# Optimization experiments

Measured on AMD Instinct MI355X. Metric: run time of the kernel, lower is better.

## Reference

```python
import jax, jax.numpy as jnp
import numpy as np

CHUNK = 1024  # mirrors torch chunk_size; keeps per-step intermediate bounded


def _chunked_min_dist(source, target):
    # source: [N, d], target: [M, d] -> [N] min squared distance to target
    n, d = source.shape
    chunks = source.reshape(n // CHUNK, CHUNK, d)

    def step(chunk):
        # diff: [CHUNK, M, d]; dist: [CHUNK, M]
        diff = chunk[:, None, :] - target[None, :, :]
        dist = jnp.sum(diff * diff, axis=-1)
        return jnp.min(dist, axis=1)

    mins = jax.lax.map(step, chunks)  # [n//CHUNK, CHUNK]
    return mins.reshape(n)


def setup_inputs() -> dict:
    key = jax.random.key(0)
    k1, k2 = jax.random.split(key)
    pred = jax.random.normal(k1, (32768, 3), dtype=jnp.float32)
    target = jax.random.normal(k2, (32768, 3), dtype=jnp.float32)
    return {"pred": pred, "target": target}


def reference(pred, target):
    min_pred_to_target = _chunked_min_dist(pred, target)
    min_target_to_pred = _chunked_min_dist(target, pred)
    # reduction='mean'
    return min_pred_to_target.mean() + min_target_to_pred.mean()
```

## Files before the change

### kernel.cpp

```cpp
#include <hip/hip_runtime.h>

#define NPTS 32768
#define G 32
#define NCELL (G*G*G)
#define SSTR (NCELL + 1)
#define RANGE 4.5f
#define CELLW 0.28125f

typedef unsigned int u32;


__device__ __forceinline__ int cell_of(float v) {
    int c = (int)floorf((v + RANGE) * (G / (2.0f * RANGE)));
    return min(max(c, 0), G - 1);
}
__device__ __forceinline__ float cell_lo(int i) {
    return fmaf((float)i, CELLW, -RANGE);
}

__global__ __launch_bounds__(256)
void hist_k(const float* __restrict__ pred, const float* __restrict__ targ,
            u32* __restrict__ cnt, u32* __restrict__ strag_cnt,
            float* __restrict__ out) {
    int i = blockIdx.x * 256 + threadIdx.x;
    if (i == 0) { *out = 0.0f; *strag_cnt = 0u; }
    int cloud = i >> 15, k = i & (NPTS - 1);
    const float* p = cloud ? targ : pred;
    float x = p[3*k], y = p[3*k+1], z = p[3*k+2];
    int c = (cell_of(z) * G + cell_of(y)) * G + cell_of(x);
    atomicAdd(&cnt[cloud * NCELL + c], 1u);
}

__global__ __launch_bounds__(1024)
void scan_k(const u32* __restrict__ cnt, u32* __restrict__ S, u32* __restrict__ cursor) {
    int cloud = blockIdx.x;
    const u32* c = cnt + cloud * NCELL;
    u32* s   = S + cloud * SSTR;
    u32* cur = cursor + cloud * NCELL;
    __shared__ u32 wt[16];
    int t = threadIdx.x, lane = t & 63, wave = t >> 6;

    u32 loc[32], run = 0;
    #pragma unroll
    for (int k = 0; k < 32; ++k) { loc[k] = run; run += c[32 * t + k]; }
    u32 inc = run;
    #pragma unroll
    for (int off = 1; off < 64; off <<= 1) {
        u32 nv = __shfl_up(inc, off, 64);
        if (lane >= off) inc += nv;
    }
    if (lane == 63) wt[wave] = inc;
    __syncthreads();
    if (t == 0) {
        u32 a = 0;
        #pragma unroll
        for (int w = 0; w < 16; ++w) { u32 v = wt[w]; wt[w] = a; a += v; }
    }
    __syncthreads();
    u32 tb = wt[wave] + (inc - run);
    #pragma unroll
    for (int k = 0; k < 32; ++k) {
        u32 v = tb + loc[k];
        s[32 * t + k] = v; cur[32 * t + k] = v;
    }
    if (t == 1023) s[NCELL] = NPTS;
}

__global__ __launch_bounds__(256)
void scatter_k(const float* __restrict__ pred, const float* __restrict__ targ,
               u32* __restrict__ cursor,
               float4* __restrict__ sortedA, float4* __restrict__ sortedB) {
    int i = blockIdx.x * 256 + threadIdx.x;
    int cloud = i >> 15, k = i & (NPTS - 1);
    const float* p = cloud ? targ : pred;
    float x = p[3*k], y = p[3*k+1], z = p[3*k+2];
    int c = (cell_of(z) * G + cell_of(y)) * G + cell_of(x);
    u32 pos = atomicAdd(&cursor[cloud * NCELL + c], 1u);
    (cloud ? sortedB : sortedA)[pos] = make_float4(x, y, z, 0.0f);
}

__device__ __forceinline__ float box_bound(int cx, int cy, int cz, float4 q, int R) {
    float bd = 3.4e38f;
    if (cx - R > 0)     bd = fminf(bd, q.x - cell_lo(cx - R));
    if (cx + R < G - 1) bd = fminf(bd, cell_lo(cx + R + 1) - q.x);
    if (cy - R > 0)     bd = fminf(bd, q.y - cell_lo(cy - R));
    if (cy + R < G - 1) bd = fminf(bd, cell_lo(cy + R + 1) - q.y);
    if (cz - R > 0)     bd = fminf(bd, q.z - cell_lo(cz - R));
    if (cz + R < G - 1) bd = fminf(bd, cell_lo(cz + R + 1) - q.z);
    return bd;
}

__global__ __launch_bounds__(256, 8)
void query_dense(const float4* __restrict__ sortedA, const float4* __restrict__ sortedB,
                 const u32* __restrict__ Sall, u32* __restrict__ strag_cnt,
                 u32* __restrict__ strag_list, float* __restrict__ out) {
    int tid = blockIdx.x * 256 + threadIdx.x;
    int sub = tid & 7;
    int qi = tid >> 3;
    int cloud = qi >> 15, k = qi & (NPTS - 1);
    const float4* Q = cloud ? sortedB : sortedA;
    const float4* T = cloud ? sortedA : sortedB;
    const u32* s = Sall + (cloud ^ 1) * SSTR;

    float4 q = Q[k];
    int cx = cell_of(q.x), cy = cell_of(q.y), cz = cell_of(q.z);
    int x0 = max(cx - 1, 0), x1 = min(cx + 1, G - 1);
    float best = 3.4e38f;

    int cbc = (cz * G + cy) * G;
    u32 cbeg = s[cbc + x0], cend = s[cbc + x1 + 1];
    u32 rb[9], re[9];
    #pragma unroll
    for (int i = 0; i < 9; ++i) {
        int dy = (i % 3) - 1, dz = (i / 3) - 1;
        int Y = cy + dy, Z = cz + dz;
        rb[i] = 0; re[i] = 0;
        if (i != 4 && (unsigned)Y < G && (unsigned)Z < G) {
            int cb = (Z * G + Y) * G;
            rb[i] = s[cb + x0]; re[i] = s[cb + x1 + 1];
        }
    }

    auto scan_seg = [&](u32 beg, u32 end) {
        for (u32 e = beg + sub; e < end; e += 8) {
            float4 t = T[e];
            float dx = q.x - t.x, dy = q.y - t.y, dz = q.z - t.z;
            best = fminf(best, fmaf(dx, dx, fmaf(dy, dy, dz * dz)));
        }
    };
    auto group_min = [&]() {
        best = fminf(best, __shfl_xor(best, 1, 64));
        best = fminf(best, __shfl_xor(best, 2, 64));
        best = fminf(best, __shfl_xor(best, 4, 64));
    };

    scan_seg(cbeg, cend);
    group_min();

    #pragma unroll
    for (int i = 0; i < 9; ++i) {
        if (i == 4) continue;
        int dy = (i % 3) - 1, dz = (i / 3) - 1;
        int Y = cy + dy, Z = cz + dz;
        if ((unsigned)Y >= G || (unsigned)Z >= G) continue;
        float ey = dy > 0 ? cell_lo(Y) - q.y : q.y - cell_lo(Y + 1);
        float ez = dz > 0 ? cell_lo(Z) - q.z : q.z - cell_lo(Z + 1);
        if (dy == 0) ey = 0.0f;
        if (dz == 0) ez = 0.0f;
        float mind2 = fmaf(ey, ey, ez * ez);
        if (mind2 < best) scan_seg(rb[i], re[i]);
    }
    group_min();

    float bd = box_bound(cx, cy, cz, q, 1);
    if (best > bd * bd) {
        if (sub == 0) {
            u32 slot = atomicAdd(strag_cnt, 1u);
            strag_list[slot] = (u32)qi;
        }
        best = 0.0f;
    }

    float v = best * 0.125f;
    #pragma unroll
    for (int off = 1; off < 64; off <<= 1)
        v += __shfl_xor(v, off, 64);
    __shared__ float wsum[4];
    int lane = threadIdx.x & 63, wave = threadIdx.x >> 6;
    if (lane == 0) wsum[wave] = v;
    __syncthreads();
    if (threadIdx.x == 0)
        atomicAdd(out, (wsum[0] + wsum[1] + wsum[2] + wsum[3]) * (1.0f / NPTS));
}

__global__ __launch_bounds__(256, 8)
void query_strag(const float4* __restrict__ sortedA, const float4* __restrict__ sortedB,
                 const u32* __restrict__ Sall, const u32* __restrict__ strag_cnt,
                 const u32* __restrict__ strag_list, float* __restrict__ out) {
    u32 n = *strag_cnt;
    int lane = threadIdx.x & 63;
    u32 wid = (blockIdx.x * 256 + threadIdx.x) >> 6;
    u32 nw = (gridDim.x * 256) >> 6;

    for (u32 idx = wid; idx < n; idx += nw) {
        u32 qi = strag_list[idx];
        int cloud = qi >> 15, k = qi & (NPTS - 1);
        const float4* Q = cloud ? sortedB : sortedA;
        const float4* T = cloud ? sortedA : sortedB;
        const u32* s = Sall + (cloud ^ 1) * SSTR;

        float4 q = Q[k];
        int cx = cell_of(q.x), cy = cell_of(q.y), cz = cell_of(q.z);
        int xlo = max(cx - 4, 0), xhi = min(cx + 4, G - 1);
        float best = 3.4e38f;

        u32 rb0 = 0, re0 = 0, rb1 = 0, re1 = 0;
        {
            int Z = cz + lane / 9 - 4, Y = cy + lane % 9 - 4;
            if ((unsigned)Z < G && (unsigned)Y < G) {
                int cb = (Z * G + Y) * G;
                rb0 = s[cb + xlo]; re0 = s[cb + xhi + 1];
            }
        }
        if (lane < 17) {
            int ri = lane + 64;
            int Z = cz + ri / 9 - 4, Y = cy + ri % 9 - 4;
            if ((unsigned)Z < G && (unsigned)Y < G) {
                int cb = (Z * G + Y) * G;
                rb1 = s[cb + xlo]; re1 = s[cb + xhi + 1];
            }
        }
        for (u32 e = rb0; e < re0; ++e) {
            float4 t = T[e];
            float dx = q.x - t.x, dy = q.y - t.y, dz = q.z - t.z;
            best = fminf(best, fmaf(dx, dx, fmaf(dy, dy, dz * dz)));
        }
        for (u32 e = rb1; e < re1; ++e) {
            float4 t = T[e];
            float dx = q.x - t.x, dy = q.y - t.y, dz = q.z - t.z;
            best = fminf(best, fmaf(dx, dx, fmaf(dy, dy, dz * dz)));
        }
        #pragma unroll
        for (int off = 1; off < 64; off <<= 1)
            best = fminf(best, __shfl_xor(best, off, 64));

        float bd4 = box_bound(cx, cy, cz, q, 4);
        if (best > bd4 * bd4) {
            auto d2 = [&](float4 t) {
                float dx = q.x - t.x, dy = q.y - t.y, dz = q.z - t.z;
                return fmaf(dx, dx, fmaf(dy, dy, dz * dz));
            };
            float a0 = 3.4e38f, a1 = 3.4e38f, a2 = 3.4e38f, a3 = 3.4e38f;
            #pragma unroll 2
            for (int blk = 0; blk < NPTS / 512; ++blk) {
                u32 base = (u32)lane + (u32)blk * 512u;
                float4 t0 = T[base];
                float4 t1 = T[base + 64];
                float4 t2 = T[base + 128];
                float4 t3 = T[base + 192];
                float4 t4 = T[base + 256];
                float4 t5 = T[base + 320];
                float4 t6 = T[base + 384];
                float4 t7 = T[base + 448];
                a0 = fminf(a0, d2(t0)); a1 = fminf(a1, d2(t1));
                a2 = fminf(a2, d2(t2)); a3 = fminf(a3, d2(t3));
                a0 = fminf(a0, d2(t4)); a1 = fminf(a1, d2(t5));
                a2 = fminf(a2, d2(t6)); a3 = fminf(a3, d2(t7));
            }
            float bb = fminf(fminf(a0, a1), fminf(a2, a3));
            #pragma unroll
            for (int off = 1; off < 64; off <<= 1)
                bb = fminf(bb, __shfl_xor(bb, off, 64));
            best = fminf(best, bb);
        }

        if (lane == 0) atomicAdd(out, best * (1.0f / NPTS));
    }
}

extern "C" void kernel_launch(void* const* d_in, const int* in_sizes, int n_in,
                              void* d_out, int out_size, void* d_ws, size_t ws_size,
                              hipStream_t stream) {
    const float* pred = (const float*)d_in[0];
    const float* targ = (const float*)d_in[1];
    float* out = (float*)d_out;
    char* ws = (char*)d_ws;
    float4* sortedA = (float4*)(ws);
    float4* sortedB = (float4*)(ws + (512 << 10));
    u32* S         = (u32*)(ws + (1024 << 10));
    u32* cnt       = (u32*)(ws + (1344 << 10));
    u32* cursor    = (u32*)(ws + (1600 << 10));
    u32* strag_cnt = (u32*)(ws + (1856 << 10));
    u32* strag_list = cnt;

    hipMemsetAsync(cnt, 0, 2 * NCELL * sizeof(u32), stream);
    hist_k     <<<256, 256, 0, stream>>>(pred, targ, cnt, strag_cnt, out);
    scan_k     <<<2, 1024, 0, stream>>>(cnt, S, cursor);
    scatter_k  <<<256, 256, 0, stream>>>(pred, targ, cursor, sortedA, sortedB);
    query_dense<<<2048, 256, 0, stream>>>(sortedA, sortedB, S, strag_cnt, strag_list, out);
    query_strag<<<512, 256, 0, stream>>>(sortedA, sortedB, S, strag_cnt, strag_list, out);
}
```

Measured before the change: 150.4 us.

## Use half-norm dot-product distance form and unroll neighbor scan by four

Stores half the squared norm in the w component of each sorted point, so the dense query compares 0.5|t|^2 - q·t (three FMAs) instead of computing a full squared difference. The segment scan is unrolled to issue four independent loads per iteration with clamped indices and masking, which raises memory-level parallelism. Pruning and straggler tests are rewritten in the shifted metric, and the final distance is recovered as 2*(hb + q.w), clamped at zero. The expanded-norm form can lose precision through cancellation for nearby points, and the clamped extra loads cost some wasted bandwidth.

```diff
diff --git a/kernel.cpp b/kernel.cpp
--- a/kernel.cpp
+++ b/kernel.cpp
@@ -76,7 +76,8 @@
     float x = p[3*k], y = p[3*k+1], z = p[3*k+2];
     int c = (cell_of(z) * G + cell_of(y)) * G + cell_of(x);
     u32 pos = atomicAdd(&cursor[cloud * NCELL + c], 1u);
-    (cloud ? sortedB : sortedA)[pos] = make_float4(x, y, z, 0.0f);
+    (cloud ? sortedB : sortedA)[pos] =
+        make_float4(x, y, z, 0.5f * fmaf(x, x, fmaf(y, y, z * z)));
 }
 
 __device__ __forceinline__ float box_bound(int cx, int cy, int cz, float4 q, int R) {
@@ -105,7 +106,7 @@
     float4 q = Q[k];
     int cx = cell_of(q.x), cy = cell_of(q.y), cz = cell_of(q.z);
     int x0 = max(cx - 1, 0), x1 = min(cx + 1, G - 1);
-    float best = 3.4e38f;
+    float hb = 3.4e38f;
 
     int cbc = (cz * G + cy) * G;
     u32 cbeg = s[cbc + x0], cend = s[cbc + x1 + 1];
@@ -121,17 +122,27 @@
         }
     }
 
+    auto hval = [&](float4 t) {
+        return fmaf(-q.x, t.x, fmaf(-q.y, t.y, fmaf(-q.z, t.z, t.w)));
+    };
     auto scan_seg = [&](u32 beg, u32 end) {
-        for (u32 e = beg + sub; e < end; e += 8) {
-            float4 t = T[e];
-            float dx = q.x - t.x, dy = q.y - t.y, dz = q.z - t.z;
-            best = fminf(best, fmaf(dx, dx, fmaf(dy, dy, dz * dz)));
+        for (u32 e = beg + sub; e < end; e += 32) {
+            u32 e1 = min(e + 8u,  (u32)NPTS - 1);
+            u32 e2 = min(e + 16u, (u32)NPTS - 1);
+            u32 e3 = min(e + 24u, (u32)NPTS - 1);
+            float4 t0 = T[e];  float4 t1 = T[e1];
+            float4 t2 = T[e2]; float4 t3 = T[e3];
+            float h0 = hval(t0);
+            float h1 = (e + 8u  < end) ? hval(t1) : 3.4e38f;
+            float h2 = (e + 16u < end) ? hval(t2) : 3.4e38f;
+            float h3 = (e + 24u < end) ? hval(t3) : 3.4e38f;
+            hb = fminf(hb, fminf(fminf(h0, h1), fminf(h2, h3)));
         }
     };
     auto group_min = [&]() {
-        best = fminf(best, __shfl_xor(best, 1, 64));
-        best = fminf(best, __shfl_xor(best, 2, 64));
-        best = fminf(best, __shfl_xor(best, 4, 64));
+        hb = fminf(hb, __shfl_xor(hb, 1, 64));
+        hb = fminf(hb, __shfl_xor(hb, 2, 64));
+        hb = fminf(hb, __shfl_xor(hb, 4, 64));
     };
 
     scan_seg(cbeg, cend);
@@ -148,17 +159,20 @@
         if (dy == 0) ey = 0.0f;
         if (dz == 0) ez = 0.0f;
         float mind2 = fmaf(ey, ey, ez * ez);
-        if (mind2 < best) scan_seg(rb[i], re[i]);
+        if (fmaf(0.5f, mind2, -q.w) < hb) scan_seg(rb[i], re[i]);
     }
     group_min();
 
     float bd = box_bound(cx, cy, cz, q, 1);
-    if (best > bd * bd) {
+    float best;
+    if (hb > fmaf(0.5f * bd, bd, -q.w)) {
         if (sub == 0) {
             u32 slot = atomicAdd(strag_cnt, 1u);
             strag_list[slot] = (u32)qi;
         }
         best = 0.0f;
+    } else {
+        best = fmaxf(fmaf(2.0f, hb, 2.0f * q.w), 0.0f);
     }
 
     float v = best * 0.125f;
@@ -234,14 +248,10 @@
             #pragma unroll 2
             for (int blk = 0; blk < NPTS / 512; ++blk) {
                 u32 base = (u32)lane + (u32)blk * 512u;
-                float4 t0 = T[base];
-                float4 t1 = T[base + 64];
-                float4 t2 = T[base + 128];
-                float4 t3 = T[base + 192];
-                float4 t4 = T[base + 256];
-                float4 t5 = T[base + 320];
-                float4 t6 = T[base + 384];
-                float4 t7 = T[base + 448];
+                float4 t0 = T[base];       float4 t1 = T[base + 64];
+                float4 t2 = T[base + 128]; float4 t3 = T[base + 192];
+                float4 t4 = T[base + 256]; float4 t5 = T[base + 320];
+                float4 t6 = T[base + 384]; float4 t7 = T[base + 448];
                 a0 = fminf(a0, d2(t0)); a1 = fminf(a1, d2(t1));
                 a2 = fminf(a2, d2(t2)); a3 = fminf(a3, d2(t3));
                 a0 = fminf(a0, d2(t4)); a1 = fminf(a1, d2(t5));
```

Result: slower. 220.7 us (+46.7%).
